# Performance work log

Measured on AMD Instinct MI355X. Metric: run time of the kernel, lower is better.

The kernel has to match this reference:

```python
import jax, jax.numpy as jnp
import numpy as np

B, T, H, N = 4, 2048, 1024, 16
DT_MIN, DT_MAX = 1e-3, 1e-1
A_INIT_MIN, A_INIT_MAX = 0.5, 2.0


def _inv_softplus(x):
    # log(exp(x) - 1), numerically stable
    return x + jnp.log(-jnp.expm1(-x))


def setup_inputs() -> dict:
    key = jax.random.key(0)
    kx, ka, kb, kc, kw, kdt = jax.random.split(key, 6)
    x = jax.random.normal(kx, (B, T, H), dtype=jnp.float32)
    A_log = jax.random.uniform(ka, (H, N), minval=np.log(A_INIT_MIN), maxval=np.log(A_INIT_MAX), dtype=jnp.float32)
    B_mat = 0.02 * jax.random.normal(kb, (H, N), dtype=jnp.float32)
    C_mat = 0.02 * jax.random.normal(kc, (H, N), dtype=jnp.float32)
    D_vec = jnp.ones((H,), dtype=jnp.float32)
    W_dt = 0.02 * jax.random.normal(kw, (H, H), dtype=jnp.float32)
    b_dt = _inv_softplus(jax.random.uniform(kdt, (H,), minval=DT_MIN, maxval=DT_MAX, dtype=jnp.float32))
    return {"x": x, "A_log": A_log, "B_mat": B_mat, "C_mat": C_mat, "D_vec": D_vec, "W_dt": W_dt, "b_dt": b_dt}


def reference(x, A_log, B_mat, C_mat, D_vec, W_dt, b_dt):
    # in_proj is Identity since input_size == hidden_size
    u = x  # (B, T, H)
    A = -jnp.exp(A_log)  # (H, N)
    # dt for all timesteps at once: softplus(u @ W_dt^T + b_dt) -> (B, T, H)
    dt = jax.nn.softplus(jnp.einsum('bth,gh->btg', u, W_dt) + b_dt)
    state0 = jnp.zeros((u.shape[0], A_log.shape[0], A_log.shape[1]), dtype=u.dtype)

    def step(state, inp):
        dt_t, u_t = inp  # (B, H), (B, H)
        dtA = dt_t[..., None]  # (B, H, 1)
        A_bar = jnp.exp(dtA * A)                       # (B, H, N)
        state = A_bar * state + (dtA * B_mat) * u_t[..., None]
        y_t = jnp.einsum('bhn,hn->bh', state, C_mat) + D_vec * u_t
        return state, y_t

    # scan over time axis
    state_final, ys = jax.lax.scan(step, state0, (dt.transpose(1, 0, 2), u.transpose(1, 0, 2)))
    out = ys.transpose(1, 0, 2)  # (B, T, H)
    return out, state_final
```

## Files before the change

kernel.cpp:

```cpp
#include <hip/hip_runtime.h>
#include <stdint.h>

#define BB 4
#define TT 2048
#define HH 1024
#define NN 16
#define KK 1024
#define GG 1024
#define MM (BB*TT)
#define NCHUNK 64
#define TC (TT/NCHUNK)
#define HB 256

#if __has_builtin(__builtin_amdgcn_exp2f)
#define FAST_EXP2(x) __builtin_amdgcn_exp2f(x)
#else
#define FAST_EXP2(x) __expf((x) * 0.6931471805599453f)
#endif
#define EXPSCALE 1.4426950408889634f

typedef __attribute__((ext_vector_type(8))) short short8;
typedef __attribute__((ext_vector_type(4))) float f32x4;

__device__ __forceinline__ unsigned short f2bf(float f) {
  union { float f; unsigned u; } a; a.f = f;
  unsigned u = a.u;
  u += 0x7fffu + ((u >> 16) & 1u);
  return (unsigned short)(u >> 16);
}

__device__ __forceinline__ unsigned pack_half2(float a, float b) {
  union { _Float16 h[2]; unsigned u; } p;
  p.h[0] = (_Float16)a; p.h[1] = (_Float16)b;
  return p.u;
}

__global__ __launch_bounds__(256) void cvt2_f32_bf16(const float* __restrict__ srcA,
                                                     unsigned short* __restrict__ dstA, int n4a,
                                                     const float* __restrict__ srcB,
                                                     unsigned short* __restrict__ dstB, int n4b) {
  int i = blockIdx.x * blockDim.x + threadIdx.x;
  const float* s; unsigned short* d; int j;
  if (i < n4a) { s = srcA; d = dstA; j = i; }
  else         { s = srcB; d = dstB; j = i - n4a; if (j >= n4b) return; }
  float4 a = ((const float4*)s)[j];
  ushort4 o;
  o.x = f2bf(a.x); o.y = f2bf(a.y); o.z = f2bf(a.z); o.w = f2bf(a.w);
  ((ushort4*)d)[j] = o;
}

__global__ __launch_bounds__(256, 4) void gemm_dt(const unsigned short* __restrict__ xb,
                                                  const unsigned short* __restrict__ wb,
                                                  const float* __restrict__ b_dt,
                                                  _Float16* __restrict__ dtH) {
  __shared__ short lsA[128 * 64];
  __shared__ short lsB[64 * 64];
  const int tid  = threadIdx.x;
  const int w    = tid >> 6;
  const int lane = tid & 63;
  const int bid  = blockIdx.x;
  const int swz  = (bid & 7) * 128 + (bid >> 3);
  const int m0 = (swz >> 4) * 128;
  const int g0 = (swz & 15) * 64;

  const int r8 = lane >> 3;
  const int c8 = (lane & 7) * 8;
  const unsigned short* gA[4];
  short*                lA[4];
#pragma unroll
  for (int q = 0; q < 4; ++q) {
    const int row = w * 32 + q * 8 + r8;
    gA[q] = xb + (size_t)(m0 + row) * KK + c8;
    lA[q] = lsA + row * 64;
  }
  const unsigned short* gB[2];
  short*                lB[2];
#pragma unroll
  for (int q = 0; q < 2; ++q) {
    const int row = w * 16 + q * 8 + r8;
    gB[q] = wb + (size_t)(g0 + row) * KK + c8;
    lB[q] = lsB + row * 64;
  }

  const int wm   = (w >> 1) * 64;
  const int wg   = (w & 1) * 32;
  const int lrow = lane & 15;
  const int lq   = lane >> 4;

  int aoff[4][2], boff[2][2];
#pragma unroll
  for (int mi = 0; mi < 4; ++mi) {
    const int row = wm + mi * 16 + lrow;
    aoff[mi][0] = row * 64 + lq * 8;
    aoff[mi][1] = row * 64 + 32 + lq * 8;
  }
#pragma unroll
  for (int ni = 0; ni < 2; ++ni) {
    const int row = wg + ni * 16 + lrow;
    boff[ni][0] = row * 64 + lq * 8;
    boff[ni][1] = row * 64 + 32 + lq * 8;
  }

  f32x4 acc[4][2];
  const f32x4 zero = {0.f, 0.f, 0.f, 0.f};
#pragma unroll
  for (int i = 0; i < 4; ++i)
#pragma unroll
    for (int j = 0; j < 2; ++j) acc[i][j] = zero;

  for (int kt = 0; kt < KK / 64; ++kt) {
    const int ko = kt * 64;
#pragma unroll
    for (int q = 0; q < 4; ++q)
      __builtin_amdgcn_global_load_lds((__attribute__((address_space(1))) void*)(gA[q] + ko),
                                       (__attribute__((address_space(3))) void*)(lA[q]), 16, 0, 0);
#pragma unroll
    for (int q = 0; q < 2; ++q)
      __builtin_amdgcn_global_load_lds((__attribute__((address_space(1))) void*)(gB[q] + ko),
                                       (__attribute__((address_space(3))) void*)(lB[q]), 16, 0, 0);
    __syncthreads();

#pragma unroll
    for (int kk = 0; kk < 2; ++kk) {
      short8 af[4], bfr[2];
#pragma unroll
      for (int mi = 0; mi < 4; ++mi) af[mi] = *(const short8*)&lsA[aoff[mi][kk]];
#pragma unroll
      for (int ni = 0; ni < 2; ++ni) bfr[ni] = *(const short8*)&lsB[boff[ni][kk]];
#pragma unroll
      for (int mi = 0; mi < 4; ++mi)
#pragma unroll
        for (int ni = 0; ni < 2; ++ni)
          acc[mi][ni] = __builtin_amdgcn_mfma_f32_16x16x32_bf16(af[mi], bfr[ni], acc[mi][ni], 0, 0, 0);
    }
    __syncthreads();
  }

  const int mrow = m0 + wm + lq * 4;
#pragma unroll
  for (int ni = 0; ni < 2; ++ni) {
    const int g = g0 + wg + ni * 16 + lrow;
    const float bias = b_dt[g];
#pragma unroll
    for (int mi = 0; mi < 4; ++mi)
#pragma unroll
      for (int r = 0; r < 4; ++r) {
        float z = acc[mi][ni][r] + bias;
        dtH[(size_t)(mrow + mi * 16 + r) * GG + g] =
            (_Float16)(fmaxf(z, 0.f) + __logf(1.f + __expf(-fabsf(z))));
      }
  }
}

__device__ __forceinline__ void p1_load8(const float* __restrict__ up,
                                         const _Float16* __restrict__ dp, int t0,
                                         float (&U)[8], _Float16 (&D)[8]) {
#pragma unroll
  for (int i = 0; i < 8; ++i) {
    U[i] = up[(size_t)(t0 + i) * HH];
    D[i] = dp[(size_t)(t0 + i) * HH];
  }
}

__device__ __forceinline__ void p1_comp8(const float (&U)[8], const _Float16 (&D)[8], int t0,
                                         float (&s)[NN], float& sd,
                                         const float (&Ae)[NN], const float (&Cb)[NN],
                                         float Dv, unsigned* __restrict__ yp) {
#pragma unroll
  for (int i = 0; i < 8; ++i) {
    const float dtv = (float)D[i];
    const float uv  = U[i];
    const float du  = dtv * uv;
    sd += dtv;
    float y0 = Dv * uv, y1 = 0.f, y2 = 0.f, y3 = 0.f;
#pragma unroll
    for (int n = 0; n < NN; n += 4) {
      float ab;
      ab = FAST_EXP2(dtv * Ae[n]);     s[n]     = fmaf(ab, s[n],     du); y0 = fmaf(Cb[n],     s[n],     y0);
      ab = FAST_EXP2(dtv * Ae[n + 1]); s[n + 1] = fmaf(ab, s[n + 1], du); y1 = fmaf(Cb[n + 1], s[n + 1], y1);
      ab = FAST_EXP2(dtv * Ae[n + 2]); s[n + 2] = fmaf(ab, s[n + 2], du); y2 = fmaf(Cb[n + 2], s[n + 2], y2);
      ab = FAST_EXP2(dtv * Ae[n + 3]); s[n + 3] = fmaf(ab, s[n + 3], du); y3 = fmaf(Cb[n + 3], s[n + 3], y3);
    }
    yp[(size_t)(t0 + i) * HH] = pack_half2((y0 + y1) + (y2 + y3), sd);
  }
}

__global__ __launch_bounds__(256, 4) void ssm_phase1(const float* __restrict__ x,
                                                     const _Float16* __restrict__ dtH,
                                                     const float* __restrict__ A_log,
                                                     const float* __restrict__ Bm_,
                                                     const float* __restrict__ Cm_,
                                                     const float* __restrict__ Dv_,
                                                     float* __restrict__ sloc,
                                                     float* __restrict__ sdArr,
                                                     unsigned* __restrict__ ylsd) {
  const int tid = threadIdx.x;
  const int bid = blockIdx.x;
  const int hb = bid & (HH / HB - 1);
  const int b  = (bid >> 2) & (BB - 1);
  const int c  = bid >> 4;
  const int h  = hb * HB + tid;

  const size_t base = ((size_t)b * TT + c * TC) * HH + h;
  const float*    up = x + base;
  const _Float16* dp = dtH + base;
  unsigned*       yp = ylsd + base;

  float Ae[NN], Cb[NN];
#pragma unroll
  for (int n = 0; n < NN; ++n) {
    Ae[n] = -__expf(A_log[h * NN + n]) * EXPSCALE;
    Cb[n] = Cm_[h * NN + n] * Bm_[h * NN + n];
  }
  const float Dv = Dv_[h];

  float s[NN];
#pragma unroll
  for (int n = 0; n < NN; ++n) s[n] = 0.f;
  float sd = 0.f;

  float Ua[8], Ub[8];
  _Float16 Da[8], Db[8];
  p1_load8(up, dp, 0, Ua, Da);
  p1_load8(up, dp, 8, Ub, Db);
  p1_comp8(Ua, Da, 0, s, sd, Ae, Cb, Dv, yp);
  p1_load8(up, dp, 16, Ua, Da);
  p1_comp8(Ub, Db, 8, s, sd, Ae, Cb, Dv, yp);
  p1_load8(up, dp, 24, Ub, Db);
  p1_comp8(Ua, Da, 16, s, sd, Ae, Cb, Dv, yp);
  p1_comp8(Ub, Db, 24, s, sd, Ae, Cb, Dv, yp);

  float* sp = sloc + (((size_t)c * BB + b) * HH + h) * NN;
#pragma unroll
  for (int n = 0; n < NN; n += 4) {
    f32x4 v = {s[n], s[n + 1], s[n + 2], s[n + 3]};
    *(f32x4*)&sp[n] = v;
  }
  sdArr[((size_t)c * BB + b) * HH + h] = sd;
}

__global__ __launch_bounds__(256) void ssm_phase2(float* __restrict__ sloc,
                                                  const float* __restrict__ sdArr,
                                                  const float* __restrict__ A_log,
                                                  const float* __restrict__ Bm_,
                                                  float* __restrict__ stateOut) {
  const int id = blockIdx.x * 256 + threadIdx.x;
  const int hn = id & (HH * NN - 1);
  const int bh = id >> 4;
  const float Ae = -__expf(A_log[hn]) * EXPSCALE;
  float carry = 0.f;
#pragma unroll 4
  for (int ch = 0; ch < NCHUNK; ++ch) {
    const size_t idx = (size_t)ch * (BB * HH * NN) + id;
    const float sl = sloc[idx];
    const float dc = FAST_EXP2(Ae * sdArr[(size_t)ch * (BB * HH) + bh]);
    sloc[idx] = carry;
    carry = fmaf(dc, carry, sl);
  }
  stateOut[id] = Bm_[hn] * carry;
}

__device__ __forceinline__ void p3_load8(const unsigned* __restrict__ yp, int t0,
                                         unsigned (&V)[8]) {
#pragma unroll
  for (int i = 0; i < 8; ++i) V[i] = yp[(size_t)(t0 + i) * HH];
}

__device__ __forceinline__ void p3_comp8(const unsigned (&V)[8], int t0,
                                         const float (&Ae)[NN], const float (&cc)[NN],
                                         float* __restrict__ yo) {
#pragma unroll
  for (int i = 0; i < 8; ++i) {
    union { unsigned u; _Float16 hh[2]; } q; q.u = V[i];
    const float sdv = (float)q.hh[1];
    float y0 = (float)q.hh[0], y1 = 0.f, y2 = 0.f, y3 = 0.f;
#pragma unroll
    for (int n = 0; n < NN; n += 4) {
      y0 = fmaf(cc[n],     FAST_EXP2(Ae[n]     * sdv), y0);
      y1 = fmaf(cc[n + 1], FAST_EXP2(Ae[n + 1] * sdv), y1);
      y2 = fmaf(cc[n + 2], FAST_EXP2(Ae[n + 2] * sdv), y2);
      y3 = fmaf(cc[n + 3], FAST_EXP2(Ae[n + 3] * sdv), y3);
    }
    yo[(size_t)(t0 + i) * HH] = (y0 + y1) + (y2 + y3);
  }
}

__global__ __launch_bounds__(256, 4) void ssm_phase3(const unsigned* __restrict__ ylsd,
                                                     const float* __restrict__ A_log,
                                                     const float* __restrict__ Bm_,
                                                     const float* __restrict__ Cm_,
                                                     const float* __restrict__ carryBuf,
                                                     float* __restrict__ out) {
  const int tid = threadIdx.x;
  const int bid = blockIdx.x;
  const int hb = bid & (HH / HB - 1);
  const int b  = (bid >> 2) & (BB - 1);
  const int c  = bid >> 4;
  const int h  = hb * HB + tid;

  const size_t base = ((size_t)b * TT + c * TC) * HH + h;
  const unsigned* yp = ylsd + base;
  float*          yo = out + base;

  float Ae[NN], cc[NN];
#pragma unroll
  for (int n = 0; n < NN; ++n) Ae[n] = -__expf(A_log[h * NN + n]) * EXPSCALE;

  const float* cp = carryBuf + (((size_t)c * BB + b) * HH + h) * NN;
#pragma unroll
  for (int n = 0; n < NN; n += 4) {
    f32x4 v = *(const f32x4*)&cp[n];
#pragma unroll
    for (int q = 0; q < 4; ++q)
      cc[n + q] = Cm_[h * NN + n + q] * Bm_[h * NN + n + q] * v[q];
  }

  unsigned Va[8], Vb[8];
  p3_load8(yp, 0, Va);
  p3_load8(yp, 8, Vb);
  p3_comp8(Va, 0, Ae, cc, yo);
  p3_load8(yp, 16, Va);
  p3_comp8(Vb, 8, Ae, cc, yo);
  p3_load8(yp, 24, Vb);
  p3_comp8(Va, 16, Ae, cc, yo);
  p3_comp8(Vb, 24, Ae, cc, yo);
}

extern "C" void kernel_launch(void* const* d_in, const int* in_sizes, int n_in,
                              void* d_out, int out_size, void* d_ws, size_t ws_size,
                              hipStream_t stream) {
  const float* x     = (const float*)d_in[0];
  const float* A_log = (const float*)d_in[1];
  const float* B_mat = (const float*)d_in[2];
  const float* C_mat = (const float*)d_in[3];
  const float* D_vec = (const float*)d_in[4];
  const float* W_dt  = (const float*)d_in[5];
  const float* b_dt  = (const float*)d_in[6];
  float* out = (float*)d_out;

  char* ws = (char*)d_ws;
  unsigned short* xb   = (unsigned short*)(ws);
  unsigned short* wb   = (unsigned short*)(ws + 16777216);
  _Float16*       dtH  = (_Float16*)(ws + 18874368);
  unsigned*       ylsd = (unsigned*)(ws + 35651584);
  float*          sloc  = (float*)(ws);
  float*          sdArr = (float*)(ws + 16777216);
  float* stateOut = out + (size_t)BB * TT * HH;

  const int n4x = MM * KK / 4, n4w = GG * KK / 4;
  cvt2_f32_bf16<<<(n4x + n4w + 255) / 256, 256, 0, stream>>>(x, xb, n4x, W_dt, wb, n4w);
  gemm_dt<<<(MM / 128) * (GG / 64), 256, 0, stream>>>(xb, wb, b_dt, dtH);

  const int nblk = (HH / HB) * BB * NCHUNK;
  ssm_phase1<<<nblk, 256, 0, stream>>>(x, dtH, A_log, B_mat, C_mat, D_vec, sloc, sdArr, ylsd);
  ssm_phase2<<<(BB * HH * NN) / 256, 256, 0, stream>>>(sloc, sdArr, A_log, B_mat, stateOut);
  ssm_phase3<<<nblk, 256, 0, stream>>>(ylsd, A_log, B_mat, C_mat, sloc, out);
}
```

Baseline: 191.7 us.

## Recompute chunk scan in phase3 with carry-in and split state across lane pairs

Phase1 now only computes the local chunk end-state and summed dt. It no longer writes per-step partial outputs and cumulative dt to an intermediate buffer. Phase3 reruns the recurrence from the carried-in state, producing exact outputs and removing the fp16 ylsd round trip. Each head's 16 state elements are split across two lanes 32 apart and combined with a shuffle, which halves registers per thread and doubles the block count. The cost is redoing the exp-heavy recurrence in phase3 and re-reading x and dt, in exchange for less memory traffic and higher occupancy.

```diff
diff --git a/kernel.cpp b/kernel.cpp
--- a/kernel.cpp
+++ b/kernel.cpp
@@ -10,7 +10,6 @@
 #define MM (BB*TT)
 #define NCHUNK 64
 #define TC (TT/NCHUNK)
-#define HB 256
 
 #if __has_builtin(__builtin_amdgcn_exp2f)
 #define FAST_EXP2(x) __builtin_amdgcn_exp2f(x)
@@ -27,12 +26,6 @@
   unsigned u = a.u;
   u += 0x7fffu + ((u >> 16) & 1u);
   return (unsigned short)(u >> 16);
-}
-
-__device__ __forceinline__ unsigned pack_half2(float a, float b) {
-  union { _Float16 h[2]; unsigned u; } p;
-  p.h[0] = (_Float16)a; p.h[1] = (_Float16)b;
-  return p.u;
 }
 
 __global__ __launch_bounds__(256) void cvt2_f32_bf16(const float* __restrict__ srcA,
@@ -152,91 +145,68 @@
   }
 }
 
-__device__ __forceinline__ void p1_load8(const float* __restrict__ up,
-                                         const _Float16* __restrict__ dp, int t0,
-                                         float (&U)[8], _Float16 (&D)[8]) {
-#pragma unroll
-  for (int i = 0; i < 8; ++i) {
-    U[i] = up[(size_t)(t0 + i) * HH];
-    D[i] = dp[(size_t)(t0 + i) * HH];
-  }
-}
-
-__device__ __forceinline__ void p1_comp8(const float (&U)[8], const _Float16 (&D)[8], int t0,
-                                         float (&s)[NN], float& sd,
-                                         const float (&Ae)[NN], const float (&Cb)[NN],
-                                         float Dv, unsigned* __restrict__ yp) {
-#pragma unroll
-  for (int i = 0; i < 8; ++i) {
-    const float dtv = (float)D[i];
-    const float uv  = U[i];
-    const float du  = dtv * uv;
-    sd += dtv;
-    float y0 = Dv * uv, y1 = 0.f, y2 = 0.f, y3 = 0.f;
-#pragma unroll
-    for (int n = 0; n < NN; n += 4) {
-      float ab;
-      ab = FAST_EXP2(dtv * Ae[n]);     s[n]     = fmaf(ab, s[n],     du); y0 = fmaf(Cb[n],     s[n],     y0);
-      ab = FAST_EXP2(dtv * Ae[n + 1]); s[n + 1] = fmaf(ab, s[n + 1], du); y1 = fmaf(Cb[n + 1], s[n + 1], y1);
-      ab = FAST_EXP2(dtv * Ae[n + 2]); s[n + 2] = fmaf(ab, s[n + 2], du); y2 = fmaf(Cb[n + 2], s[n + 2], y2);
-      ab = FAST_EXP2(dtv * Ae[n + 3]); s[n + 3] = fmaf(ab, s[n + 3], du); y3 = fmaf(Cb[n + 3], s[n + 3], y3);
-    }
-    yp[(size_t)(t0 + i) * HH] = pack_half2((y0 + y1) + (y2 + y3), sd);
-  }
-}
-
-__global__ __launch_bounds__(256, 4) void ssm_phase1(const float* __restrict__ x,
+
+__global__ __launch_bounds__(256, 8) void ssm_phase1(const float* __restrict__ x,
                                                      const _Float16* __restrict__ dtH,
                                                      const float* __restrict__ A_log,
-                                                     const float* __restrict__ Bm_,
-                                                     const float* __restrict__ Cm_,
-                                                     const float* __restrict__ Dv_,
                                                      float* __restrict__ sloc,
-                                                     float* __restrict__ sdArr,
-                                                     unsigned* __restrict__ ylsd) {
+                                                     float* __restrict__ sdArr) {
   const int tid = threadIdx.x;
+  const int hl  = ((tid >> 6) << 5) + (tid & 31);
+  const int nh  = (tid >> 5) & 1;
   const int bid = blockIdx.x;
-  const int hb = bid & (HH / HB - 1);
-  const int b  = (bid >> 2) & (BB - 1);
-  const int c  = bid >> 4;
-  const int h  = hb * HB + tid;
+  const int hb = bid & 7;
+  const int b  = (bid >> 3) & (BB - 1);
+  const int c  = bid >> 5;
+  const int h  = hb * 128 + hl;
 
   const size_t base = ((size_t)b * TT + c * TC) * HH + h;
   const float*    up = x + base;
   const _Float16* dp = dtH + base;
-  unsigned*       yp = ylsd + base;
-
-  float Ae[NN], Cb[NN];
-#pragma unroll
-  for (int n = 0; n < NN; ++n) {
-    Ae[n] = -__expf(A_log[h * NN + n]) * EXPSCALE;
-    Cb[n] = Cm_[h * NN + n] * Bm_[h * NN + n];
-  }
-  const float Dv = Dv_[h];
-
-  float s[NN];
-#pragma unroll
-  for (int n = 0; n < NN; ++n) s[n] = 0.f;
+
+  float Ae[8];
+  {
+    f32x4 a0 = *(const f32x4*)&A_log[h * NN + nh * 8];
+    f32x4 a1 = *(const f32x4*)&A_log[h * NN + nh * 8 + 4];
+#pragma unroll
+    for (int q = 0; q < 4; ++q) {
+      Ae[q]     = -__expf(a0[q]) * EXPSCALE;
+      Ae[q + 4] = -__expf(a1[q]) * EXPSCALE;
+    }
+  }
+
+  float s[8];
+#pragma unroll
+  for (int q = 0; q < 8; ++q) s[q] = 0.f;
   float sd = 0.f;
 
-  float Ua[8], Ub[8];
-  _Float16 Da[8], Db[8];
-  p1_load8(up, dp, 0, Ua, Da);
-  p1_load8(up, dp, 8, Ub, Db);
-  p1_comp8(Ua, Da, 0, s, sd, Ae, Cb, Dv, yp);
-  p1_load8(up, dp, 16, Ua, Da);
-  p1_comp8(Ub, Db, 8, s, sd, Ae, Cb, Dv, yp);
-  p1_load8(up, dp, 24, Ub, Db);
-  p1_comp8(Ua, Da, 16, s, sd, Ae, Cb, Dv, yp);
-  p1_comp8(Ub, Db, 24, s, sd, Ae, Cb, Dv, yp);
-
-  float* sp = sloc + (((size_t)c * BB + b) * HH + h) * NN;
-#pragma unroll
-  for (int n = 0; n < NN; n += 4) {
-    f32x4 v = {s[n], s[n + 1], s[n + 2], s[n + 3]};
-    *(f32x4*)&sp[n] = v;
-  }
-  sdArr[((size_t)c * BB + b) * HH + h] = sd;
+#pragma unroll
+  for (int j = 0; j < TC / 8; ++j) {
+    float uu[8], dv[8];
+#pragma unroll
+    for (int i = 0; i < 8; ++i) {
+      uu[i] = up[(size_t)(j * 8 + i) * HH];
+      dv[i] = (float)dp[(size_t)(j * 8 + i) * HH];
+    }
+#pragma unroll
+    for (int i = 0; i < 8; ++i) {
+      const float dtv = dv[i];
+      const float du  = dtv * uu[i];
+      sd += dtv;
+#pragma unroll
+      for (int q = 0; q < 8; ++q) {
+        const float ab = FAST_EXP2(dtv * Ae[q]);
+        s[q] = fmaf(ab, s[q], du);
+      }
+    }
+  }
+
+  float* sp = sloc + (((size_t)c * BB + b) * HH + h) * NN + nh * 8;
+  f32x4 v0 = {s[0], s[1], s[2], s[3]};
+  f32x4 v1 = {s[4], s[5], s[6], s[7]};
+  *(f32x4*)&sp[0] = v0;
+  *(f32x4*)&sp[4] = v1;
+  if (nh == 0) sdArr[((size_t)c * BB + b) * HH + h] = sd;
 }
 
 __global__ __launch_bounds__(256) void ssm_phase2(float* __restrict__ sloc,
@@ -260,70 +230,80 @@
   stateOut[id] = Bm_[hn] * carry;
 }
 
-__device__ __forceinline__ void p3_load8(const unsigned* __restrict__ yp, int t0,
-                                         unsigned (&V)[8]) {
-#pragma unroll
-  for (int i = 0; i < 8; ++i) V[i] = yp[(size_t)(t0 + i) * HH];
-}
-
-__device__ __forceinline__ void p3_comp8(const unsigned (&V)[8], int t0,
-                                         const float (&Ae)[NN], const float (&cc)[NN],
-                                         float* __restrict__ yo) {
-#pragma unroll
-  for (int i = 0; i < 8; ++i) {
-    union { unsigned u; _Float16 hh[2]; } q; q.u = V[i];
-    const float sdv = (float)q.hh[1];
-    float y0 = (float)q.hh[0], y1 = 0.f, y2 = 0.f, y3 = 0.f;
-#pragma unroll
-    for (int n = 0; n < NN; n += 4) {
-      y0 = fmaf(cc[n],     FAST_EXP2(Ae[n]     * sdv), y0);
-      y1 = fmaf(cc[n + 1], FAST_EXP2(Ae[n + 1] * sdv), y1);
-      y2 = fmaf(cc[n + 2], FAST_EXP2(Ae[n + 2] * sdv), y2);
-      y3 = fmaf(cc[n + 3], FAST_EXP2(Ae[n + 3] * sdv), y3);
-    }
-    yo[(size_t)(t0 + i) * HH] = (y0 + y1) + (y2 + y3);
-  }
-}
-
-__global__ __launch_bounds__(256, 4) void ssm_phase3(const unsigned* __restrict__ ylsd,
+__global__ __launch_bounds__(256, 8) void ssm_phase3(const float* __restrict__ x,
+                                                     const _Float16* __restrict__ dtH,
                                                      const float* __restrict__ A_log,
                                                      const float* __restrict__ Bm_,
                                                      const float* __restrict__ Cm_,
+                                                     const float* __restrict__ Dv_,
                                                      const float* __restrict__ carryBuf,
                                                      float* __restrict__ out) {
   const int tid = threadIdx.x;
+  const int hl  = ((tid >> 6) << 5) + (tid & 31);
+  const int nh  = (tid >> 5) & 1;
   const int bid = blockIdx.x;
-  const int hb = bid & (HH / HB - 1);
-  const int b  = (bid >> 2) & (BB - 1);
-  const int c  = bid >> 4;
-  const int h  = hb * HB + tid;
+  const int hb = bid & 7;
+  const int b  = (bid >> 3) & (BB - 1);
+  const int c  = bid >> 5;
+  const int h  = hb * 128 + hl;
 
   const size_t base = ((size_t)b * TT + c * TC) * HH + h;
-  const unsigned* yp = ylsd + base;
+  const float*    up = x + base;
+  const _Float16* dp = dtH + base;
   float*          yo = out + base;
 
-  float Ae[NN], cc[NN];
-#pragma unroll
-  for (int n = 0; n < NN; ++n) Ae[n] = -__expf(A_log[h * NN + n]) * EXPSCALE;
-
-  const float* cp = carryBuf + (((size_t)c * BB + b) * HH + h) * NN;
-#pragma unroll
-  for (int n = 0; n < NN; n += 4) {
-    f32x4 v = *(const f32x4*)&cp[n];
-#pragma unroll
-    for (int q = 0; q < 4; ++q)
-      cc[n + q] = Cm_[h * NN + n + q] * Bm_[h * NN + n + q] * v[q];
-  }
-
-  unsigned Va[8], Vb[8];
-  p3_load8(yp, 0, Va);
-  p3_load8(yp, 8, Vb);
-  p3_comp8(Va, 0, Ae, cc, yo);
-  p3_load8(yp, 16, Va);
-  p3_comp8(Vb, 8, Ae, cc, yo);
-  p3_load8(yp, 24, Vb);
-  p3_comp8(Va, 16, Ae, cc, yo);
-  p3_comp8(Vb, 24, Ae, cc, yo);
+  float Ae[8], Cb[8];
+  {
+    f32x4 a0 = *(const f32x4*)&A_log[h * NN + nh * 8];
+    f32x4 a1 = *(const f32x4*)&A_log[h * NN + nh * 8 + 4];
+    f32x4 c0 = *(const f32x4*)&Cm_[h * NN + nh * 8];
+    f32x4 c1 = *(const f32x4*)&Cm_[h * NN + nh * 8 + 4];
+    f32x4 b0 = *(const f32x4*)&Bm_[h * NN + nh * 8];
+    f32x4 b1 = *(const f32x4*)&Bm_[h * NN + nh * 8 + 4];
+#pragma unroll
+    for (int q = 0; q < 4; ++q) {
+      Ae[q]     = -__expf(a0[q]) * EXPSCALE;
+      Ae[q + 4] = -__expf(a1[q]) * EXPSCALE;
+      Cb[q]     = c0[q] * b0[q];
+      Cb[q + 4] = c1[q] * b1[q];
+    }
+  }
+  const float Dv = (nh == 0) ? Dv_[h] : 0.f;
+
+  float s[8];
+  {
+    const float* cp = carryBuf + (((size_t)c * BB + b) * HH + h) * NN + nh * 8;
+    f32x4 v0 = *(const f32x4*)&cp[0];
+    f32x4 v1 = *(const f32x4*)&cp[4];
+#pragma unroll
+    for (int q = 0; q < 4; ++q) { s[q] = v0[q]; s[q + 4] = v1[q]; }
+  }
+
+#pragma unroll
+  for (int j = 0; j < TC / 8; ++j) {
+    float uu[8], dv[8];
+#pragma unroll
+    for (int i = 0; i < 8; ++i) {
+      uu[i] = up[(size_t)(j * 8 + i) * HH];
+      dv[i] = (float)dp[(size_t)(j * 8 + i) * HH];
+    }
+#pragma unroll
+    for (int i = 0; i < 8; ++i) {
+      const float dtv = dv[i];
+      const float uv  = uu[i];
+      const float du  = dtv * uv;
+      float y0 = Dv * uv, y1 = 0.f;
+#pragma unroll
+      for (int q = 0; q < 8; q += 2) {
+        float ab;
+        ab = FAST_EXP2(dtv * Ae[q]);     s[q]     = fmaf(ab, s[q],     du); y0 = fmaf(Cb[q],     s[q],     y0);
+        ab = FAST_EXP2(dtv * Ae[q + 1]); s[q + 1] = fmaf(ab, s[q + 1], du); y1 = fmaf(Cb[q + 1], s[q + 1], y1);
+      }
+      float y = y0 + y1;
+      y += __shfl_xor(y, 32);
+      if (nh == 0) yo[(size_t)(j * 8 + i) * HH] = y;
+    }
+  }
 }
 
 extern "C" void kernel_launch(void* const* d_in, const int* in_sizes, int n_in,
@@ -342,7 +322,6 @@
   unsigned short* xb   = (unsigned short*)(ws);
   unsigned short* wb   = (unsigned short*)(ws + 16777216);
   _Float16*       dtH  = (_Float16*)(ws + 18874368);
-  unsigned*       ylsd = (unsigned*)(ws + 35651584);
   float*          sloc  = (float*)(ws);
   float*          sdArr = (float*)(ws + 16777216);
   float* stateOut = out + (size_t)BB * TT * HH;
@@ -351,8 +330,8 @@
   cvt2_f32_bf16<<<(n4x + n4w + 255) / 256, 256, 0, stream>>>(x, xb, n4x, W_dt, wb, n4w);
   gemm_dt<<<(MM / 128) * (GG / 64), 256, 0, stream>>>(xb, wb, b_dt, dtH);
 
-  const int nblk = (HH / HB) * BB * NCHUNK;
-  ssm_phase1<<<nblk, 256, 0, stream>>>(x, dtH, A_log, B_mat, C_mat, D_vec, sloc, sdArr, ylsd);
+  const int nblk = (HH / 128) * BB * NCHUNK;
+  ssm_phase1<<<nblk, 256, 0, stream>>>(x, dtH, A_log, sloc, sdArr);
   ssm_phase2<<<(BB * HH * NN) / 256, 256, 0, stream>>>(sloc, sdArr, A_log, B_mat, stateOut);
-  ssm_phase3<<<nblk, 256, 0, stream>>>(ylsd, A_log, B_mat, C_mat, sloc, out);
-}
+  ssm_phase3<<<nblk, 256, 0, stream>>>(x, dtH, A_log, B_mat, C_mat, D_vec, sloc, out);
+}
```

After: 209.5 us. 9.3% more time.
